# Optimization experiments

Hardware: AMD Instinct MI355X
Metric: run time of the kernel (lower is better)

The kernel has to match this reference:

```python
import jax, jax.numpy as jnp
import numpy as np

TOP_K = 2  # config.num_active_experts


def setup_inputs() -> dict:
    key = jax.random.key(0)
    k1, k2, k3, k4 = jax.random.split(key, 4)
    B, S, D = 2, 2048, 1024
    E, W = 8, 1024  # 8 experts, each width 1024 -> total_expert_width = 8192
    x = jax.random.normal(k1, (B, S, D), dtype=jnp.float32)
    router_w = jax.random.normal(k2, (E, D), dtype=jnp.float32) * 0.02
    w1 = jax.random.normal(k3, (D, E * W), dtype=jnp.float32) * 0.02
    w2 = jax.random.normal(k4, (E * W, D), dtype=jnp.float32) * 0.02
    return {"x": x, "router_w": router_w, "w1": w1, "w2": w2}


def reference(x, router_w, w1, w2):
    B, S, D = x.shape
    E = router_w.shape[0]
    W = w1.shape[1] // E  # uniform expert width
    T = B * S
    xf = x.reshape(T, D)

    # Router: sigmoid gating, top-k, sum-normalized weights (norm_topk_prob)
    router_logits = jnp.einsum('td,ed->te', xf, router_w)
    router_probs = jax.nn.sigmoid(router_logits.astype(jnp.float32))
    top_w, sel = jax.lax.top_k(router_probs, TOP_K)          # [T,K]
    top_w = top_w / (top_w.sum(axis=-1, keepdims=True) + 1e-20)
    top_w = top_w.astype(x.dtype)

    # Expert MLPs: expert e uses w1[:, off_e:off_e+W], w2[off_e:off_e+W, :].
    # Uniform width -> single batched einsum over experts (same math as the
    # padded-gather / block-sparse SDD/DSD grouped GEMM pipeline).
    W1e = w1.reshape(D, E, W).transpose(1, 0, 2)             # [E,D,W]
    W2e = w2.reshape(E, W, D)                                # [E,W,D]
    h = jnp.einsum('td,edw->etw', xf, W1e)                   # up-proj
    a = jnp.square(jax.nn.relu(h))                           # relu_squared
    y = jnp.einsum('etw,ewd->etd', a, W2e)                   # down-proj

    # Weighted scatter-combine: combine_weights[t,e] = top_w if e selected else 0
    cw = jnp.zeros((T, E), dtype=x.dtype).at[jnp.arange(T)[:, None], sel].set(top_w)
    out = jnp.einsum('etd,te->td', y, cw)
    return out.reshape(B, S, D)
```

## Files before the change

kernel.cpp:

```cpp
#include <hip/hip_runtime.h>
#include <hip/hip_bf16.h>


#define T_TOKENS 4096
#define DD 1024
#define EE 8
#define WW 1024
#define CAP 1536
#define BM 128
#define BN 128
#define BK 64
#define MT (CAP / BM)
#define NT (WW / BN)
#define GEMM_BLOCKS (EE * MT * NT)
#define TR1_BLOCKS 512
#define TR2_BLOCKS 512
#define TLD 132

typedef short bf16x8 __attribute__((ext_vector_type(8)));
typedef float f32x4 __attribute__((ext_vector_type(4)));

__device__ __forceinline__ void gload_lds16(const void* g, void* l) {
  __builtin_amdgcn_global_load_lds((__attribute__((address_space(1))) void*)(g),
                                   (__attribute__((address_space(3))) void*)(l),
                                   16, 0, 0);
}

__device__ __forceinline__ float bf2f(unsigned short u) {
  union { unsigned int i; float f; } v; v.i = (unsigned int)u << 16; return v.f;
}

__device__ __forceinline__ unsigned short f2bf_u(float f) {
  __hip_bfloat16 h = __float2bfloat16(f);
  union { __hip_bfloat16 h; unsigned short u; } c; c.h = h; return c.u;
}

__device__ __forceinline__ void transpose_tile_128(
    const float* __restrict__ src, long src_ld, long r0, long c0,
    unsigned short* __restrict__ dst, long dst_ld, unsigned short* lds)
{
  int tid = threadIdx.x;
  int cq = tid & 31;
  int rb = tid >> 5;
#pragma unroll
  for (int i = 0; i < 16; i++) {
    int r = rb + i * 8;
    f32x4 v = *(const f32x4*)(src + (r0 + r) * src_ld + c0 + cq * 4);
#pragma unroll
    for (int j = 0; j < 4; j++)
      lds[(cq * 4 + j) * TLD + r] = f2bf_u(v[j]);
  }
  __syncthreads();
#pragma unroll
  for (int it = 0; it < 8; it++) {
    int slot = it * 256 + tid;
    int c = slot >> 4;
    int m = slot & 15;
    const unsigned short* p = lds + (size_t)c * TLD + m * 8;
    uint2 lo = *(const uint2*)(p);
    uint2 hi = *(const uint2*)(p + 4);
    uint4 o; o.x = lo.x; o.y = lo.y; o.z = hi.x; o.w = hi.y;
    *(uint4*)(dst + (c0 + c) * dst_ld + r0 + m * 8) = o;
  }
}

__global__ __launch_bounds__(256) void pre_kernel(
    const float* __restrict__ w1, const float* __restrict__ x,
    const float* __restrict__ rw,
    __hip_bfloat16* __restrict__ w1t, __hip_bfloat16* __restrict__ xb,
    int* __restrict__ sel, float* __restrict__ wpair)
{
  __shared__ unsigned short lds_t[128 * TLD];
  int b = blockIdx.x;
  if (b < TR1_BLOCKS) {
    int bn = b >> 3;
    int bd = b & 7;
    transpose_tile_128(w1, EE * WW, (long)bd * 128, (long)bn * 128,
                       (unsigned short*)w1t, DD, lds_t);
  } else {
    int lane = threadIdx.x & 63;
    int wave = threadIdx.x >> 6;
    int t = (b - TR1_BLOCKS) * 4 + wave;
    const float* xrow = x + (size_t)t * DD;
    float acc[EE];
#pragma unroll
    for (int e = 0; e < EE; e++) acc[e] = 0.f;
#pragma unroll
    for (int i = 0; i < DD / 64; i++) {
      int d = lane + i * 64;
      float xv = xrow[d];
      xb[t * DD + d] = __float2bfloat16(xv);
#pragma unroll
      for (int e = 0; e < EE; e++) acc[e] += xv * rw[e * DD + d];
    }
#pragma unroll
    for (int e = 0; e < EE; e++) {
#pragma unroll
      for (int off = 32; off > 0; off >>= 1)
        acc[e] += __shfl_down(acc[e], off, 64);
    }
    if (lane == 0) {
      float p[EE];
#pragma unroll
      for (int e = 0; e < EE; e++) p[e] = 1.f / (1.f + expf(-acc[e]));
      int e0 = 0; float b0 = p[0];
      for (int e = 1; e < EE; e++) if (p[e] > b0) { b0 = p[e]; e0 = e; }
      int e1 = -1; float b1 = -1.f;
      for (int e = 0; e < EE; e++) {
        if (e == e0) continue;
        if (p[e] > b1) { b1 = p[e]; e1 = e; }
      }
      float s = b0 + b1 + 1e-20f;
      sel[t] = e0 | (e1 << 8);
      wpair[2 * t]     = b0 / s;
      wpair[2 * t + 1] = b1 / s;
    }
  }
}

__global__ __launch_bounds__(1024) void build_lists(
    const int* __restrict__ sel, int* __restrict__ counts,
    int* __restrict__ idx, int* __restrict__ tslot)
{
  __shared__ int lcnt[EE];
  int tid = threadIdx.x, lane = tid & 63;
  if (tid < EE) lcnt[tid] = 0;
  __syncthreads();
  unsigned long long lower = (1ull << lane) - 1;
#pragma unroll
  for (int j = 0; j < T_TOKENS / 1024; j++) {
    int t = j * 1024 + tid;
    int s = sel[t];
    int e0 = s & 0xff, e1 = (s >> 8) & 0xff;
    int slot0 = 0, slot1 = 0;
#pragma unroll
    for (int e = 0; e < EE; e++) {
      unsigned long long m0 = __ballot(e0 == e);
      unsigned long long m1 = __ballot(e1 == e);
      int c0 = __popcll(m0), c1 = __popcll(m1);
      int base = 0;
      if (lane == 0 && (c0 + c1) > 0) base = atomicAdd(&lcnt[e], c0 + c1);
      base = __shfl(base, 0, 64);
      if (e0 == e) slot0 = base + __popcll(m0 & lower);
      if (e1 == e) slot1 = base + c0 + __popcll(m1 & lower);
    }
    int p0 = e0 * CAP + slot0, p1 = e1 * CAP + slot1;
    idx[p0] = t; idx[p1] = t;
    tslot[2 * t] = p0; tslot[2 * t + 1] = p1;
  }
  __syncthreads();
  if (tid < EE) counts[tid] = lcnt[tid];
}

__global__ __launch_bounds__(256, 3) void gemm1_kernel(
    const __hip_bfloat16* __restrict__ xb, const __hip_bfloat16* __restrict__ w1t,
    const int* __restrict__ counts, const int* __restrict__ idx,
    __hip_bfloat16* __restrict__ act,
    const float* __restrict__ w2, __hip_bfloat16* __restrict__ w2t)
{
  __shared__ __attribute__((aligned(16))) char smem[128 * TLD * 2];
  int bid = blockIdx.x;
  if (bid >= GEMM_BLOCKS) {
    int z = bid - GEMM_BLOCKS;
    int e = z >> 6;
    int t2 = z & 63;
    int bw = t2 >> 3;
    int bdd = t2 & 7;
    transpose_tile_128(w2 + (long)e * WW * DD, DD,
                       (long)bw * 128, (long)bdd * 128,
                       (unsigned short*)(w2t + (long)e * DD * WW), WW,
                       (unsigned short*)smem);
    return;
  }
  short* As = (short*)smem;
  short* Bs = (short*)(smem + 16384);
  int e = bid & 7;
  int i = bid >> 3;
  int mt = i >> 3, nt = i & 7;
  int n_e = counts[e];
  if (mt * BM >= n_e) return;

  int tid = threadIdx.x;
  int lane = tid & 63;
  int wave = __builtin_amdgcn_readfirstlane(tid >> 6);
  int wm = (wave >> 1) * 64, wn = (wave & 1) * 64;
  int m16 = lane & 15, qd = lane >> 4;

  const __hip_bfloat16* gA[4];
  const __hip_bfloat16* gB[4];
#pragma unroll
  for (int i2 = 0; i2 < 4; i2++) {
    int s = i2 * 256 + tid;
    int r = s >> 3;
    int q = (s & 7) ^ (r & 7);
    int rowA = mt * BM + r;
    int slot = rowA < n_e ? rowA : n_e - 1;
    int tok = idx[e * CAP + slot];
    gA[i2] = xb + (size_t)tok * DD + q * 8;
    gB[i2] = w1t + ((size_t)e * WW + nt * BN + r) * DD + q * 8;
  }
  short* ldsA[4];
  short* ldsB[4];
#pragma unroll
  for (int i2 = 0; i2 < 4; i2++) {
    ldsA[i2] = As + (i2 * 256 + wave * 64) * 8;
    ldsB[i2] = Bs + (i2 * 256 + wave * 64) * 8;
  }

  int aoff[4][2], boff[4][2];
#pragma unroll
  for (int mi = 0; mi < 4; mi++) {
    int r = wm + mi * 16 + m16;
#pragma unroll
    for (int h = 0; h < 2; h++)
      aoff[mi][h] = (r * 8 + ((qd + h * 4) ^ (r & 7))) * 8;
  }
#pragma unroll
  for (int ni = 0; ni < 4; ni++) {
    int r = wn + ni * 16 + m16;
#pragma unroll
    for (int h = 0; h < 2; h++)
      boff[ni][h] = (r * 8 + ((qd + h * 4) ^ (r & 7))) * 8;
  }

  f32x4 zero = {0.f, 0.f, 0.f, 0.f};
  f32x4 acc[4][4];
#pragma unroll
  for (int mi = 0; mi < 4; mi++)
#pragma unroll
    for (int ni = 0; ni < 4; ni++) acc[mi][ni] = zero;

  for (int k0 = 0; k0 < DD; k0 += BK) {
#pragma unroll
    for (int i2 = 0; i2 < 4; i2++) gload_lds16(gA[i2] + k0, ldsA[i2]);
#pragma unroll
    for (int i2 = 0; i2 < 4; i2++) gload_lds16(gB[i2] + k0, ldsB[i2]);
    __syncthreads();
#pragma unroll
    for (int h = 0; h < 2; h++) {
      bf16x8 af[4], bfr[4];
#pragma unroll
      for (int mi = 0; mi < 4; mi++) af[mi] = *(const bf16x8*)(As + aoff[mi][h]);
#pragma unroll
      for (int ni = 0; ni < 4; ni++) bfr[ni] = *(const bf16x8*)(Bs + boff[ni][h]);
#pragma unroll
      for (int mi = 0; mi < 4; mi++)
#pragma unroll
        for (int ni = 0; ni < 4; ni++)
          acc[mi][ni] = __builtin_amdgcn_mfma_f32_16x16x32_bf16(
              af[mi], bfr[ni], acc[mi][ni], 0, 0, 0);
    }
    __syncthreads();
  }

#pragma unroll
  for (int mi = 0; mi < 4; mi++) {
#pragma unroll
    for (int reg = 0; reg < 4; reg++) {
      int rowt = mt * BM + wm + mi * 16 + qd * 4 + reg;
      if (rowt < n_e) {
#pragma unroll
        for (int ni = 0; ni < 4; ni++) {
          float v = acc[mi][ni][reg];
          v = v > 0.f ? v * v : 0.f;
          int col = nt * BN + wn + ni * 16 + m16;
          act[((size_t)e * CAP + rowt) * WW + col] = __float2bfloat16(v);
        }
      }
    }
  }
}

__global__ __launch_bounds__(256, 3) void gemm2_kernel(
    const __hip_bfloat16* __restrict__ act, const __hip_bfloat16* __restrict__ w2t,
    const int* __restrict__ counts, __hip_bfloat16* __restrict__ y)
{
  __shared__ __attribute__((aligned(16))) char smem[32768];
  short* As = (short*)smem;
  short* Bs = (short*)(smem + 16384);
  int bid = blockIdx.x;
  int e = bid & 7;
  int i = bid >> 3;
  int mt = i >> 3, nt = i & 7;
  int n_e = counts[e];
  if (mt * BM >= n_e) return;

  int tid = threadIdx.x;
  int lane = tid & 63;
  int wave = __builtin_amdgcn_readfirstlane(tid >> 6);
  int wm = (wave >> 1) * 64, wn = (wave & 1) * 64;
  int m16 = lane & 15, qd = lane >> 4;

  const __hip_bfloat16* gA[4];
  const __hip_bfloat16* gB[4];
#pragma unroll
  for (int i2 = 0; i2 < 4; i2++) {
    int s = i2 * 256 + tid;
    int r = s >> 3;
    int q = (s & 7) ^ (r & 7);
    gA[i2] = act + ((size_t)e * CAP + mt * BM + r) * WW + q * 8;
    gB[i2] = w2t + ((size_t)e * DD + nt * BN + r) * WW + q * 8;
  }
  short* ldsA[4];
  short* ldsB[4];
#pragma unroll
  for (int i2 = 0; i2 < 4; i2++) {
    ldsA[i2] = As + (i2 * 256 + wave * 64) * 8;
    ldsB[i2] = Bs + (i2 * 256 + wave * 64) * 8;
  }

  int aoff[4][2], boff[4][2];
#pragma unroll
  for (int mi = 0; mi < 4; mi++) {
    int r = wm + mi * 16 + m16;
#pragma unroll
    for (int h = 0; h < 2; h++)
      aoff[mi][h] = (r * 8 + ((qd + h * 4) ^ (r & 7))) * 8;
  }
#pragma unroll
  for (int ni = 0; ni < 4; ni++) {
    int r = wn + ni * 16 + m16;
#pragma unroll
    for (int h = 0; h < 2; h++)
      boff[ni][h] = (r * 8 + ((qd + h * 4) ^ (r & 7))) * 8;
  }

  f32x4 zero = {0.f, 0.f, 0.f, 0.f};
  f32x4 acc[4][4];
#pragma unroll
  for (int mi = 0; mi < 4; mi++)
#pragma unroll
    for (int ni = 0; ni < 4; ni++) acc[mi][ni] = zero;

  for (int k0 = 0; k0 < WW; k0 += BK) {
#pragma unroll
    for (int i2 = 0; i2 < 4; i2++) gload_lds16(gA[i2] + k0, ldsA[i2]);
#pragma unroll
    for (int i2 = 0; i2 < 4; i2++) gload_lds16(gB[i2] + k0, ldsB[i2]);
    __syncthreads();
#pragma unroll
    for (int h = 0; h < 2; h++) {
      bf16x8 af[4], bfr[4];
#pragma unroll
      for (int mi = 0; mi < 4; mi++) af[mi] = *(const bf16x8*)(As + aoff[mi][h]);
#pragma unroll
      for (int ni = 0; ni < 4; ni++) bfr[ni] = *(const bf16x8*)(Bs + boff[ni][h]);
#pragma unroll
      for (int mi = 0; mi < 4; mi++)
#pragma unroll
        for (int ni = 0; ni < 4; ni++)
          acc[mi][ni] = __builtin_amdgcn_mfma_f32_16x16x32_bf16(
              af[mi], bfr[ni], acc[mi][ni], 0, 0, 0);
    }
    __syncthreads();
  }

#pragma unroll
  for (int mi = 0; mi < 4; mi++) {
#pragma unroll
    for (int reg = 0; reg < 4; reg++) {
      int slot = mt * BM + wm + mi * 16 + qd * 4 + reg;
      if (slot < n_e) {
#pragma unroll
        for (int ni = 0; ni < 4; ni++) {
          int col = nt * BN + wn + ni * 16 + m16;
          y[((size_t)e * CAP + slot) * DD + col] = __float2bfloat16(acc[mi][ni][reg]);
        }
      }
    }
  }
}

__global__ __launch_bounds__(256) void combine_kernel(
    const __hip_bfloat16* __restrict__ y, const int* __restrict__ tslot,
    const float* __restrict__ wpair, float* __restrict__ out)
{
  int t = blockIdx.x;
  int c = threadIdx.x * 4;
  int s0 = tslot[2 * t], s1 = tslot[2 * t + 1];
  float w0 = wpair[2 * t], w1 = wpair[2 * t + 1];
  const unsigned short* yu = (const unsigned short*)y;
  ushort4 a = *(const ushort4*)(yu + (size_t)s0 * DD + c);
  ushort4 bq = *(const ushort4*)(yu + (size_t)s1 * DD + c);
  f32x4 o;
  o[0] = w0 * bf2f(a.x) + w1 * bf2f(bq.x);
  o[1] = w0 * bf2f(a.y) + w1 * bf2f(bq.y);
  o[2] = w0 * bf2f(a.z) + w1 * bf2f(bq.z);
  o[3] = w0 * bf2f(a.w) + w1 * bf2f(bq.w);
  *(f32x4*)(out + (size_t)t * DD + c) = o;
}

extern "C" void kernel_launch(void* const* d_in, const int* in_sizes, int n_in,
                              void* d_out, int out_size, void* d_ws, size_t ws_size,
                              hipStream_t stream)
{
  const float* x  = (const float*)d_in[0];
  const float* rw = (const float*)d_in[1];
  const float* w1 = (const float*)d_in[2];
  const float* w2 = (const float*)d_in[3];
  float* out = (float*)d_out;

  char* ws = (char*)d_ws;
  __hip_bfloat16* xb  = (__hip_bfloat16*)ws;  ws += (size_t)T_TOKENS * DD * 2;
  __hip_bfloat16* w1t = (__hip_bfloat16*)ws;  ws += (size_t)EE * WW * DD * 2;
  __hip_bfloat16* w2t = (__hip_bfloat16*)ws;  ws += (size_t)EE * DD * WW * 2;
  __hip_bfloat16* act = (__hip_bfloat16*)ws;  ws += (size_t)EE * CAP * WW * 2;
  __hip_bfloat16* y   = (__hip_bfloat16*)ws;  ws += (size_t)EE * CAP * DD * 2;
  int*   counts = (int*)ws;                   ws += 256;
  int*   idx    = (int*)ws;                   ws += (size_t)EE * CAP * 4;
  int*   sel    = (int*)ws;                   ws += (size_t)T_TOKENS * 4;
  int*   tslot  = (int*)ws;                   ws += (size_t)T_TOKENS * 8;
  float* wpair  = (float*)ws;                 ws += (size_t)T_TOKENS * 8;

  pre_kernel<<<TR1_BLOCKS + T_TOKENS / 4, 256, 0, stream>>>(
      w1, x, rw, w1t, xb, sel, wpair);
  build_lists<<<1, 1024, 0, stream>>>(sel, counts, idx, tslot);
  gemm1_kernel<<<GEMM_BLOCKS + TR2_BLOCKS, 256, 0, stream>>>(
      xb, w1t, counts, idx, act, w2, w2t);
  gemm2_kernel<<<GEMM_BLOCKS, 256, 0, stream>>>(act, w2t, counts, y);
  combine_kernel<<<T_TOKENS, 256, 0, stream>>>(y, tslot, wpair, out);
}
```

Measured before the change: 188.8 us.

## Fuse weighted combine into down-proj GEMM epilogue via atomic adds

Measured after the change: 202.5 us. +7.3%, slower.

```diff
diff --git a/kernel.cpp b/kernel.cpp
--- a/kernel.cpp
+++ b/kernel.cpp
@@ -119,8 +119,9 @@
 }
 
 __global__ __launch_bounds__(1024) void build_lists(
-    const int* __restrict__ sel, int* __restrict__ counts,
-    int* __restrict__ idx, int* __restrict__ tslot)
+    const int* __restrict__ sel, const float* __restrict__ wpair,
+    int* __restrict__ counts, int* __restrict__ idx,
+    float* __restrict__ wslot)
 {
   __shared__ int lcnt[EE];
   int tid = threadIdx.x, lane = tid & 63;
@@ -146,7 +147,8 @@
     }
     int p0 = e0 * CAP + slot0, p1 = e1 * CAP + slot1;
     idx[p0] = t; idx[p1] = t;
-    tslot[2 * t] = p0; tslot[2 * t + 1] = p1;
+    wslot[p0] = wpair[2 * t];
+    wslot[p1] = wpair[2 * t + 1];
   }
   __syncthreads();
   if (tid < EE) counts[tid] = lcnt[tid];
@@ -164,10 +166,8 @@
     int z = bid - GEMM_BLOCKS;
     int e = z >> 6;
     int t2 = z & 63;
-    int bw = t2 >> 3;
-    int bdd = t2 & 7;
     transpose_tile_128(w2 + (long)e * WW * DD, DD,
-                       (long)bw * 128, (long)bdd * 128,
+                       (long)(t2 >> 3) * 128, (long)(t2 & 7) * 128,
                        (unsigned short*)(w2t + (long)e * DD * WW), WW,
                        (unsigned short*)smem);
     return;
@@ -273,7 +273,8 @@
 
 __global__ __launch_bounds__(256, 3) void gemm2_kernel(
     const __hip_bfloat16* __restrict__ act, const __hip_bfloat16* __restrict__ w2t,
-    const int* __restrict__ counts, __hip_bfloat16* __restrict__ y)
+    const int* __restrict__ counts, const int* __restrict__ idx,
+    const float* __restrict__ wslot, float* __restrict__ out)
 {
   __shared__ __attribute__((aligned(16))) char smem[32768];
   short* As = (short*)smem;
@@ -361,33 +362,17 @@
     for (int reg = 0; reg < 4; reg++) {
       int slot = mt * BM + wm + mi * 16 + qd * 4 + reg;
       if (slot < n_e) {
+        int tok = idx[e * CAP + slot];
+        float wr = wslot[e * CAP + slot];
+        float* orow = out + (size_t)tok * DD;
 #pragma unroll
         for (int ni = 0; ni < 4; ni++) {
           int col = nt * BN + wn + ni * 16 + m16;
-          y[((size_t)e * CAP + slot) * DD + col] = __float2bfloat16(acc[mi][ni][reg]);
+          unsafeAtomicAdd(orow + col, wr * acc[mi][ni][reg]);
         }
       }
     }
   }
-}
-
-__global__ __launch_bounds__(256) void combine_kernel(
-    const __hip_bfloat16* __restrict__ y, const int* __restrict__ tslot,
-    const float* __restrict__ wpair, float* __restrict__ out)
-{
-  int t = blockIdx.x;
-  int c = threadIdx.x * 4;
-  int s0 = tslot[2 * t], s1 = tslot[2 * t + 1];
-  float w0 = wpair[2 * t], w1 = wpair[2 * t + 1];
-  const unsigned short* yu = (const unsigned short*)y;
-  ushort4 a = *(const ushort4*)(yu + (size_t)s0 * DD + c);
-  ushort4 bq = *(const ushort4*)(yu + (size_t)s1 * DD + c);
-  f32x4 o;
-  o[0] = w0 * bf2f(a.x) + w1 * bf2f(bq.x);
-  o[1] = w0 * bf2f(a.y) + w1 * bf2f(bq.y);
-  o[2] = w0 * bf2f(a.z) + w1 * bf2f(bq.z);
-  o[3] = w0 * bf2f(a.w) + w1 * bf2f(bq.w);
-  *(f32x4*)(out + (size_t)t * DD + c) = o;
 }
 
 extern "C" void kernel_launch(void* const* d_in, const int* in_sizes, int n_in,
@@ -405,18 +390,18 @@
   __hip_bfloat16* w1t = (__hip_bfloat16*)ws;  ws += (size_t)EE * WW * DD * 2;
   __hip_bfloat16* w2t = (__hip_bfloat16*)ws;  ws += (size_t)EE * DD * WW * 2;
   __hip_bfloat16* act = (__hip_bfloat16*)ws;  ws += (size_t)EE * CAP * WW * 2;
-  __hip_bfloat16* y   = (__hip_bfloat16*)ws;  ws += (size_t)EE * CAP * DD * 2;
   int*   counts = (int*)ws;                   ws += 256;
   int*   idx    = (int*)ws;                   ws += (size_t)EE * CAP * 4;
   int*   sel    = (int*)ws;                   ws += (size_t)T_TOKENS * 4;
-  int*   tslot  = (int*)ws;                   ws += (size_t)T_TOKENS * 8;
+  float* wslot  = (float*)ws;                 ws += (size_t)EE * CAP * 4;
   float* wpair  = (float*)ws;                 ws += (size_t)T_TOKENS * 8;
 
+  hipMemsetAsync(out, 0, (size_t)T_TOKENS * DD * sizeof(float), stream);
   pre_kernel<<<TR1_BLOCKS + T_TOKENS / 4, 256, 0, stream>>>(
       w1, x, rw, w1t, xb, sel, wpair);
-  build_lists<<<1, 1024, 0, stream>>>(sel, counts, idx, tslot);
+  build_lists<<<1, 1024, 0, stream>>>(sel, wpair, counts, idx, wslot);
   gemm1_kernel<<<GEMM_BLOCKS + TR2_BLOCKS, 256, 0, stream>>>(
       xb, w1t, counts, idx, act, w2, w2t);
-  gemm2_kernel<<<GEMM_BLOCKS, 256, 0, stream>>>(act, w2t, counts, y);
-  combine_kernel<<<T_TOKENS, 256, 0, stream>>>(y, tslot, wpair, out);
-}
+  gemm2_kernel<<<GEMM_BLOCKS, 256, 0, stream>>>(
+      act, w2t, counts, idx, wslot, out);
+}
```
